# Kernel tuning notes

Hardware: AMD Instinct MI355X
Metric: run time of the kernel (lower is better)

## Reference

```python
import jax, jax.numpy as jnp
import numpy as np


def _resize_axis(x, axis, out_size):
    # PyTorch bilinear interpolate, align_corners=False, no antialias (half-pixel centers)
    in_size = x.shape[axis]
    src = (jnp.arange(out_size) + 0.5) * (in_size / out_size) - 0.5
    src = jnp.clip(src, 0.0, in_size - 1.0)
    lo = jnp.floor(src).astype(jnp.int32)
    hi = jnp.minimum(lo + 1, in_size - 1)
    w = (src - lo).astype(x.dtype)
    shp = [1] * x.ndim
    shp[axis] = out_size
    w = w.reshape(shp)
    return jnp.take(x, lo, axis=axis) * (1 - w) + jnp.take(x, hi, axis=axis) * w


def _bilinear(x, h, w):
    return _resize_axis(_resize_axis(x, 2, h), 3, w)


def _unfold3(x):
    # F.unfold(kernel_size=3, padding=1) -> [B, C, 9, H*W], kernel offsets row-major
    B, C, H, W = x.shape
    xp = jnp.pad(x, ((0, 0), (0, 0), (1, 1), (1, 1)))
    pats = jnp.stack([xp[:, :, dy:dy + H, dx:dx + W] for dy in range(3) for dx in range(3)], axis=2)
    return pats.reshape(B, C, 9, H * W)


def setup_inputs() -> dict:
    key = jax.random.key(0)
    ks = jax.random.split(key, 7)
    B, C, H, W = 4, 64, 192, 192
    return {
        "x": jax.random.normal(ks[0], (B, C, H, W), jnp.float32),
        "gn_weight": jnp.ones((C,), jnp.float32) + 0.1 * jax.random.normal(ks[1], (C,), jnp.float32),
        "gn_bias": 0.1 * jax.random.normal(ks[2], (C,), jnp.float32),
        "w1": jax.random.normal(ks[3], (2 * C, C), jnp.float32) / np.sqrt(C).astype(np.float32),
        "b1": 0.01 * jax.random.normal(ks[4], (2 * C,), jnp.float32),
        "w2": jax.random.normal(ks[5], (C, 2 * C), jnp.float32) / np.sqrt(2 * C).astype(np.float32),
        "b2": 0.01 * jax.random.normal(ks[6], (C,), jnp.float32),
    }


def reference(x, gn_weight, gn_bias, w1, b1, w2, b2):
    B, C, H, W = x.shape
    MIN_CONN, MAX_CONN, THRESHOLD, POWER = 1, 16, 0.3, 2
    KSQ = 9
    K_MAX = min(MAX_CONN, KSQ)
    EPS_NORM = 1e-12

    x_down = _bilinear(x, H // 2, W // 2)
    x_du = _bilinear(x_down, H, W)
    df = jnp.abs(x - x_du).sum(1, keepdims=True)            # [B,1,H,W]
    dmin = df.reshape(B, -1).min(1).reshape(B, 1, 1, 1)
    dmax = df.reshape(B, -1).max(1).reshape(B, 1, 1, 1)
    dfp = ((df - dmin) / (dmax - dmin + 1e-8)) ** POWER
    mask = (dfp > THRESHOLD).astype(x.dtype)
    conn = MIN_CONN + jnp.clip(jnp.round(dfp * (MAX_CONN - MIN_CONN)), 0) * mask
    counts = conn.reshape(B, H * W)                          # [B,HW]
    process = counts > 1

    # ---- per-pixel cosine similarity to 3x3 neighborhood ----
    patches = _unfold3(x)                                    # [B,C,9,HW]
    x_flat = x.reshape(B, C, H * W)
    xn = x_flat / jnp.maximum(jnp.linalg.norm(x_flat, axis=1, keepdims=True), EPS_NORM)
    pn = patches / jnp.maximum(jnp.linalg.norm(patches, axis=1, keepdims=True), EPS_NORM)
    sim = jnp.einsum('bcn,bckn->bkn', xn, pn)                # [B,9,HW]

    # ---- adaptive top-k (k = min(count, 9)) + exp-softmax weighted sum of raw patches ----
    order = jnp.argsort(-sim, axis=1)                        # descending over the 9 neighbors
    sim_s = jnp.take_along_axis(sim, order, axis=1)
    pat_s = jnp.take_along_axis(patches, jnp.broadcast_to(order[:, None], patches.shape), axis=2)
    k = jnp.minimum(counts, K_MAX)                           # [B,HW]
    keep = (jnp.arange(KSQ)[None, :, None] < k[:, None, :]).astype(x.dtype)
    wts = jnp.exp(sim_s) * keep
    wts = wts / jnp.maximum(wts.sum(1, keepdims=True), EPS_NORM)
    weighted = jnp.einsum('bckn,bkn->bcn', pat_s, wts)       # [B,C,HW]
    output = jnp.where(process[:, None, :], weighted, x_flat).reshape(B, C, H, W)

    # ---- GroupNorm(32, C) on identity ----
    G = 32
    xg = x.reshape(B, G, C // G, H, W)
    mu = xg.mean((2, 3, 4), keepdims=True)
    var = xg.var((2, 3, 4), keepdims=True)
    nx = ((xg - mu) / jnp.sqrt(var + 1e-5)).reshape(B, C, H, W)
    norm_x = nx * gn_weight[None, :, None, None] + gn_bias[None, :, None, None]

    enhanced = output + norm_x
    # ---- conv_ffn: 1x1 conv C->2C, ReLU, 1x1 conv 2C->C ----
    h1 = jax.nn.relu(jnp.einsum('oc,bchw->bohw', w1, enhanced) + b1[None, :, None, None])
    ffn = jnp.einsum('oc,bchw->bohw', w2, h1) + b2[None, :, None, None]
    return enhanced + ffn
```

## Files before the change

kernel.cpp:

```cpp
#include <hip/hip_runtime.h>
#include <hip/hip_bf16.h>

#define BB 4
#define CC 64
#define HH 192
#define WW 192
#define HWSZ (HH*WW)
#define HD 96
#define WD 96
#define GG 32
#define FTH 256
#define FPX 64
#define FBPB (HWSZ/FPX)
#define PBLK 128
#define BPB (HWSZ/PBLK)

typedef short short8 __attribute__((ext_vector_type(8)));
typedef float f32x4  __attribute__((ext_vector_type(4)));

struct __align__(8) f4p { float x, y, z, w; };

__device__ __forceinline__ unsigned short f2bf(float f) {
    unsigned u = __float_as_uint(f);
    return (unsigned short)((u + 0x7FFFu + ((u >> 16) & 1u)) >> 16);
}
__device__ __forceinline__ float bf2f(unsigned short s) {
    return __uint_as_float(((unsigned)s) << 16);
}
__device__ __forceinline__ unsigned pk2(float a, float b) {
    return (unsigned)f2bf(a) | ((unsigned)f2bf(b) << 16);
}
__device__ __forceinline__ short8 u4s8(uint4 u) {
    union { uint4 a; short8 b; } cvt; cvt.a = u; return cvt.b;
}

__device__ __forceinline__ int swz1152(int bid) {
    return (bid & 7) * 144 + (bid >> 3);
}
__device__ __forceinline__ int swz2304(int bid) {
    return (bid & 7) * 288 + (bid >> 3);
}

template<int XT>
__global__ __launch_bounds__(256) void k_pre(const float* __restrict__ x,
                                             const float* __restrict__ w1,
                                             const float* __restrict__ w2,
                                             unsigned* __restrict__ wf,
                                             float* __restrict__ df,
                                             float* __restrict__ nrm,
                                             float* __restrict__ gnacc,
                                             unsigned* __restrict__ mmmin,
                                             unsigned* __restrict__ mmmax,
                                             float* __restrict__ xt) {
    __shared__ float sgn[64];
    __shared__ float wmn[4], wmx[4];
    int tid = threadIdx.x;
    if (tid < 64) sgn[tid] = 0.f;
    __syncthreads();

    if (blockIdx.x < 16) {
        #pragma unroll
        for (int rep = 0; rep < 2; ++rep) {
            int i = blockIdx.x*512 + rep*256 + tid;
            if (i < 4096) {
                float2 v = ((const float2*)w1)[i];
                int j = i >> 5, cp = i & 31, c0 = cp << 1;
                int fi = ((j >> 4) << 1) + (c0 >> 5);
                int ln = (((c0 & 31) >> 3) << 4) + (j & 15);
                wf[fi*256 + ln*4 + (cp & 3)] = pk2(v.x, v.y);
            } else {
                int i2 = i - 4096;
                float2 v = ((const float2*)w2)[i2];
                int c = i2 >> 6, jp = i2 & 63, j0 = jp << 1;
                int fi = ((j0 >> 5) << 2) + (c >> 4);
                int ln = (((j0 & 31) >> 3) << 4) + (c & 15);
                wf[4096 + fi*256 + ln*4 + (jp & 3)] = pk2(v.x, v.y);
            }
        }
    }

    int virt = swz1152(blockIdx.x);
    int b = virt / BPB;
    int pb = (virt % BPB) * PBLK;
    int wave = tid >> 6, lane = tid & 63;
    int oct = lane >> 3, grp = lane & 7;
    int p0 = pb + wave*32 + grp*4;
    int h = p0 / WW, w0 = p0 % WW;

    float hs = fminf(fmaxf(0.5f*(float)h - 0.25f, 0.f), 95.f);
    int hl = (int)hs; int hh2 = min(hl+1, 95); float fh = hs - (float)hl;
    int r0 = 2*hl, r1 = 2*hh2;

    int t0 = min(max(w0/2 - 1, 0), 92);
    float wc[4][4];
    #pragma unroll
    for (int i = 0; i < 4; ++i) {
        float wsr = fminf(fmaxf(0.5f*(float)(w0+i) - 0.25f, 0.f), 95.f);
        int wl = (int)wsr; int wh = min(wl+1, 95); float fw = wsr - (float)wl;
        int kl = wl - t0, kh = wh - t0;
        #pragma unroll
        for (int k = 0; k < 4; ++k)
            wc[i][k] = ((k==kl) ? (1.f-fw) : 0.f) + ((k==kh) ? fw : 0.f);
    }

    const float* xb = x + (size_t)b*CC*HWSZ;
    float d[4]  = {0.f,0.f,0.f,0.f};
    float qn[4] = {0.f,0.f,0.f,0.f};
    float gs[4] = {0.f,0.f,0.f,0.f};
    float gq[4] = {0.f,0.f,0.f,0.f};
    #pragma unroll
    for (int half = 0; half < 2; ++half) {
        float4 xbuf[4];
        #pragma unroll
        for (int k4 = 0; k4 < 4; ++k4) {
            int cc = half*4 + k4;
            const float* pc = xb + (size_t)(oct*8 + cc)*HWSZ;
            float4 xc = *(const float4*)(pc + h*WW + w0);
            xbuf[k4] = xc;
            const float* pa = pc + r0*WW + 2*t0;
            const float* pq = pc + r1*WW + 2*t0;
            f4p A0 = *(const f4p*)(pa);       f4p A1 = *(const f4p*)(pa + 4);
            f4p B0 = *(const f4p*)(pa + WW);  f4p B1 = *(const f4p*)(pa + WW + 4);
            f4p C0 = *(const f4p*)(pq);       f4p C1 = *(const f4p*)(pq + 4);
            f4p D0 = *(const f4p*)(pq + WW);  f4p D1 = *(const f4p*)(pq + WW + 4);
            float ra[8] = {A0.x,A0.y,A0.z,A0.w, A1.x,A1.y,A1.z,A1.w};
            float rb[8] = {B0.x,B0.y,B0.z,B0.w, B1.x,B1.y,B1.z,B1.w};
            float rc[8] = {C0.x,C0.y,C0.z,C0.w, C1.x,C1.y,C1.z,C1.w};
            float rd[8] = {D0.x,D0.y,D0.z,D0.w, D1.x,D1.y,D1.z,D1.w};
            float T[4];
            #pragma unroll
            for (int k = 0; k < 4; ++k) {
                float xdA = 0.25f*((ra[2*k] + rb[2*k]) + (ra[2*k+1] + rb[2*k+1]));
                float xdB = 0.25f*((rc[2*k] + rd[2*k]) + (rc[2*k+1] + rd[2*k+1]));
                T[k] = (1.f-fh)*xdA + fh*xdB;
            }
            float xv[4] = {xc.x, xc.y, xc.z, xc.w};
            float sch = 0.f, qch = 0.f;
            #pragma unroll
            for (int i = 0; i < 4; ++i) {
                float du = (wc[i][0]*T[0] + wc[i][1]*T[1]) + (wc[i][2]*T[2] + wc[i][3]*T[3]);
                d[i] += fabsf(xv[i] - du);
                float x2 = xv[i]*xv[i];
                qn[i] += x2;
                sch += xv[i];
                qch += x2;
            }
            gs[cc>>1] += sch;
            gq[cc>>1] += qch;
        }
        if (XT) {
            #pragma unroll
            for (int i = 0; i < 4; ++i) {
                float4 v4 = make_float4(((const float*)&xbuf[0])[i],
                                        ((const float*)&xbuf[1])[i],
                                        ((const float*)&xbuf[2])[i],
                                        ((const float*)&xbuf[3])[i]);
                *(float4*)(xt + ((size_t)b*HWSZ + p0 + i)*CC + oct*8 + half*4) = v4;
            }
        }
    }
    #pragma unroll
    for (int o = 8; o <= 32; o <<= 1) {
        #pragma unroll
        for (int i = 0; i < 4; ++i) {
            d[i]  += __shfl_xor(d[i], o);
            qn[i] += __shfl_xor(qn[i], o);
        }
    }
    if (oct == 0) {
        *(float4*)(df  + (size_t)b*HWSZ + p0) = make_float4(d[0], d[1], d[2], d[3]);
        *(float4*)(nrm + (size_t)b*HWSZ + p0) =
            make_float4(sqrtf(qn[0]), sqrtf(qn[1]), sqrtf(qn[2]), sqrtf(qn[3]));
    }
    float mn = fminf(fminf(d[0], d[1]), fminf(d[2], d[3]));
    float mx = fmaxf(fmaxf(d[0], d[1]), fmaxf(d[2], d[3]));
    #pragma unroll
    for (int o = 1; o < 64; o <<= 1) {
        mn = fminf(mn, __shfl_xor(mn, o));
        mx = fmaxf(mx, __shfl_xor(mx, o));
    }
    if (lane == 0) { wmn[wave] = mn; wmx[wave] = mx; }
    #pragma unroll
    for (int o = 1; o <= 4; o <<= 1) {
        #pragma unroll
        for (int j = 0; j < 4; ++j) {
            gs[j] += __shfl_xor(gs[j], o);
            gq[j] += __shfl_xor(gq[j], o);
        }
    }
    if (grp == 0) {
        #pragma unroll
        for (int j = 0; j < 4; ++j) {
            atomicAdd(&sgn[2*(oct*4+j)],   gs[j]);
            atomicAdd(&sgn[2*(oct*4+j)+1], gq[j]);
        }
    }
    __syncthreads();
    if (tid < 64) atomicAdd(&gnacc[(size_t)b*64 + tid], sgn[tid]);
    if (tid == 0) {
        float bmn = fminf(fminf(wmn[0], wmn[1]), fminf(wmn[2], wmn[3]));
        float bmx = fmaxf(fmaxf(wmx[0], wmx[1]), fmaxf(wmx[2], wmx[3]));
        atomicMin(&mmmin[b], __float_as_uint(bmn));
        atomicMax(&mmmax[b], __float_as_uint(bmx));
    }
}

template<int XT>
__global__ __launch_bounds__(FTH, 4) void k_fused(const float* __restrict__ x,
                                                  const float* __restrict__ xt,
                                                  const float* __restrict__ df,
                                                  const float* __restrict__ nrm,
                                                  const unsigned* __restrict__ mmmin,
                                                  const unsigned* __restrict__ mmmax,
                                                  const float* __restrict__ gnacc,
                                                  const float* __restrict__ gw,
                                                  const float* __restrict__ gb,
                                                  const unsigned* __restrict__ wf,
                                                  const float* __restrict__ b1,
                                                  const float* __restrict__ b2,
                                                  float* __restrict__ out) {
    __shared__ __align__(16) unsigned char lds[12288];
    unsigned* se = (unsigned*)lds;
    unsigned* sh = (unsigned*)(lds + 8192);
    float* gnv = (float*)(lds + 8192);

    int tid = threadIdx.x;
    int wv = tid >> 6, lane = tid & 63;
    int q = lane >> 4, m = lane & 15;

    int virt = swz2304(blockIdx.x);
    int b = virt / FBPB;
    int pb = (virt % FBPB) * FPX;
    int pxl = wv*16 + m;
    int p = pb + pxl;
    int h = p / WW, w = p % WW;
    int cbase = q*16;

    if (tid < 32) {
        float n = 2.f*HWSZ;
        float mu  = gnacc[(size_t)b*64 + 2*tid] / n;
        float var = gnacc[(size_t)b*64 + 2*tid + 1] / n - mu*mu;
        gnv[2*tid]   = mu;
        gnv[2*tid+1] = rsqrtf(var + 1e-5f);
    }
    __syncthreads();

    float dmin = __uint_as_float(mmmin[b]);
    float dmax = __uint_as_float(mmmax[b]);
    float dfp = (df[b*HWSZ+p] - dmin) / (dmax - dmin + 1e-8f);
    dfp = dfp * dfp;
    bool maskv = dfp > 0.3f;
    float conn = 1.f + (maskv ? fmaxf(rintf(dfp * 15.f), 0.f) : 0.f);
    bool process = conn > 1.f;
    int kk = (int)fminf(conn, 9.f);

    const float* xb = x + (size_t)b*CC*HWSZ + p;
    const float* pt = xt + ((size_t)b*HWSZ + p)*CC + cbase;
    const int dhv[9] = {-1,-1,-1, 0,0,0, 1,1,1};
    const int dwv[9] = {-1, 0, 1,-1,0,1,-1,0,1};
    bool valid[9]; int offc[9];
    #pragma unroll
    for (int j = 0; j < 9; ++j) {
        int hn = h + dhv[j], wn = w + dwv[j];
        valid[j] = (hn >= 0) && (hn < HH) && (wn >= 0) && (wn < WW);
        offc[j] = valid[j] ? (dhv[j]*WW + dwv[j]) : 0;
    }
    float wtc[9];
    #pragma unroll
    for (int j = 0; j < 9; ++j) wtc[j] = 0.f;

    float xa[16];
    if (XT) {
        float4 X0 = *(const float4*)(pt + 0);
        float4 X1 = *(const float4*)(pt + 4);
        float4 X2 = *(const float4*)(pt + 8);
        float4 X3 = *(const float4*)(pt + 12);
        xa[0]=X0.x;  xa[1]=X0.y;  xa[2]=X0.z;  xa[3]=X0.w;
        xa[4]=X1.x;  xa[5]=X1.y;  xa[6]=X1.z;  xa[7]=X1.w;
        xa[8]=X2.x;  xa[9]=X2.y;  xa[10]=X2.z; xa[11]=X2.w;
        xa[12]=X3.x; xa[13]=X3.y; xa[14]=X3.z; xa[15]=X3.w;
    }

    if (process) {
        float dot[9];
        if (XT) {
            #pragma unroll
            for (int j = 0; j < 9; ++j) {
                const float* nb = pt + (ptrdiff_t)offc[j]*CC;
                float4 n0 = *(const float4*)(nb + 0);
                float4 n1 = *(const float4*)(nb + 4);
                float4 n2 = *(const float4*)(nb + 8);
                float4 n3 = *(const float4*)(nb + 12);
                float na[16];
                na[0]=n0.x;  na[1]=n0.y;  na[2]=n0.z;  na[3]=n0.w;
                na[4]=n1.x;  na[5]=n1.y;  na[6]=n1.z;  na[7]=n1.w;
                na[8]=n2.x;  na[9]=n2.y;  na[10]=n2.z; na[11]=n2.w;
                na[12]=n3.x; na[13]=n3.y; na[14]=n3.z; na[15]=n3.w;
                float s = 0.f;
                #pragma unroll
                for (int cc = 0; cc < 16; ++cc)
                    s += xa[cc] * na[cc];
                dot[j] = s;
            }
        } else {
            #pragma unroll
            for (int j = 0; j < 9; ++j) dot[j] = 0.f;
            #pragma unroll 4
            for (int cc = 0; cc < 16; ++cc) {
                const float* pc = xb + (size_t)(cbase + cc)*HWSZ;
                float xc = pc[0];
                #pragma unroll
                for (int j = 0; j < 9; ++j)
                    dot[j] += xc * pc[offc[j]];
            }
        }
        #pragma unroll
        for (int j = 0; j < 9; ++j) {
            dot[j] += __shfl_xor(dot[j], 16);
            dot[j] += __shfl_xor(dot[j], 32);
        }
        float nc = fmaxf(nrm[b*HWSZ+p], 1e-12f);
        float sim[9];
        #pragma unroll
        for (int j = 0; j < 9; ++j) {
            float nj = fmaxf(nrm[b*HWSZ+p+offc[j]], 1e-12f);
            sim[j] = valid[j] ? dot[j] / (nc * nj) : 0.f;
        }
        float S = 0.f;
        float wt[9];
        #pragma unroll
        for (int j = 0; j < 9; ++j) {
            int rank = 0;
            #pragma unroll
            for (int l = 0; l < 9; ++l)
                rank += (sim[l] > sim[j]) || (sim[l] == sim[j] && l < j);
            float ex = (rank < kk) ? expf(sim[j]) : 0.f;
            wt[j] = ex; S += ex;
        }
        float inv = 1.f / fmaxf(S, 1e-12f);
        #pragma unroll
        for (int j = 0; j < 9; ++j)
            wtc[j] = valid[j] ? wt[j] * inv : 0.f;
    }

    float e[16];
    if (XT) {
        float acc[16];
        if (process) {
            #pragma unroll
            for (int cc = 0; cc < 16; ++cc) acc[cc] = 0.f;
            #pragma unroll
            for (int j = 0; j < 9; ++j) {
                const float* nb = pt + (ptrdiff_t)offc[j]*CC;
                float4 n0 = *(const float4*)(nb + 0);
                float4 n1 = *(const float4*)(nb + 4);
                float4 n2 = *(const float4*)(nb + 8);
                float4 n3 = *(const float4*)(nb + 12);
                float wj = wtc[j];
                acc[0]  += wj*n0.x;  acc[1]  += wj*n0.y;
                acc[2]  += wj*n0.z;  acc[3]  += wj*n0.w;
                acc[4]  += wj*n1.x;  acc[5]  += wj*n1.y;
                acc[6]  += wj*n1.z;  acc[7]  += wj*n1.w;
                acc[8]  += wj*n2.x;  acc[9]  += wj*n2.y;
                acc[10] += wj*n2.z;  acc[11] += wj*n2.w;
                acc[12] += wj*n3.x;  acc[13] += wj*n3.y;
                acc[14] += wj*n3.z;  acc[15] += wj*n3.w;
            }
        }
        #pragma unroll
        for (int cc = 0; cc < 16; ++cc) {
            int c = cbase + cc;
            float xc = xa[cc];
            float oc = process ? acc[cc] : xc;
            int g = c >> 1;
            float mu = gnv[2*g], is = gnv[2*g+1];
            e[cc] = oc + (xc - mu) * is * gw[c] + gb[c];
        }
    } else {
        #pragma unroll 4
        for (int cc = 0; cc < 16; ++cc) {
            int c = cbase + cc;
            const float* pc = xb + (size_t)c*HWSZ;
            float xc = pc[0];
            float oc;
            if (process) {
                float a = 0.f;
                #pragma unroll
                for (int j = 0; j < 9; ++j)
                    a += wtc[j] * pc[offc[j]];
                oc = a;
            } else oc = xc;
            int g = c >> 1;
            float mu = gnv[2*g], is = gnv[2*g+1];
            e[cc] = oc + (xc - mu) * is * gw[c] + gb[c];
        }
    }

    {
        int kc = q >> 1, qo = q & 1;
        unsigned* dst = se + (wv*2 + kc)*256;
        int la = 32*qo + m;
        uint4 ua, ub;
        ua.x = pk2(e[0],e[1]);  ua.y = pk2(e[2],e[3]);
        ua.z = pk2(e[4],e[5]);  ua.w = pk2(e[6],e[7]);
        ub.x = pk2(e[8],e[9]);  ub.y = pk2(e[10],e[11]);
        ub.z = pk2(e[12],e[13]); ub.w = pk2(e[14],e[15]);
        *(uint4*)(dst + la*4)      = ua;
        *(uint4*)(dst + (la+16)*4) = ub;
    }
    __syncthreads();

    const unsigned* wf1g = wf;
    const unsigned* wf2g = wf + 4096;
    int n16 = m;
    float b1v[8], b2v[4];
    #pragma unroll
    for (int nt = 0; nt < 8; ++nt) b1v[nt] = b1[nt*16 + n16];
    #pragma unroll
    for (int n2 = 0; n2 < 4; ++n2) b2v[n2] = b2[n2*16 + n16];

    uint4 a0 = *(uint4*)(se + (wv*2+0)*256 + lane*4);
    uint4 a1 = *(uint4*)(se + (wv*2+1)*256 + lane*4);
    f32x4 D1[8];
    #pragma unroll
    for (int nt = 0; nt < 8; ++nt) D1[nt] = (f32x4){0.f,0.f,0.f,0.f};
    #pragma unroll
    for (int nt = 0; nt < 8; ++nt) {
        uint4 bk0 = *(const uint4*)(wf1g + (nt*2+0)*256 + lane*4);
        uint4 bk1 = *(const uint4*)(wf1g + (nt*2+1)*256 + lane*4);
        D1[nt] = __builtin_amdgcn_mfma_f32_16x16x32_bf16(u4s8(a0), u4s8(bk0), D1[nt], 0, 0, 0);
        D1[nt] = __builtin_amdgcn_mfma_f32_16x16x32_bf16(u4s8(a1), u4s8(bk1), D1[nt], 0, 0, 0);
    }
    f32x4 D2[4];
    #pragma unroll
    for (int n2 = 0; n2 < 4; ++n2) D2[n2] = (f32x4){0.f,0.f,0.f,0.f};
    unsigned* shwv = sh + wv*256;
    unsigned short* shw = (unsigned short*)shwv;
    for (int kc2 = 0; kc2 < 4; ++kc2) {
        #pragma unroll
        for (int h2 = 0; h2 < 2; ++h2) {
            int nt = kc2*2 + h2;
            #pragma unroll
            for (int r = 0; r < 4; ++r) {
                float hval = fmaxf(D1[nt][r] + b1v[nt], 0.f);
                int mrow = q*4 + r;
                int k = h2*16 + n16;
                shw[((k >> 3)*16 + mrow)*8 + (k & 7)] = f2bf(hval);
            }
        }
        uint4 ah = *(uint4*)(shwv + lane*4);
        #pragma unroll
        for (int n2 = 0; n2 < 4; ++n2) {
            uint4 bb = *(const uint4*)(wf2g + (kc2*4 + n2)*256 + lane*4);
            D2[n2] = __builtin_amdgcn_mfma_f32_16x16x32_bf16(u4s8(ah), u4s8(bb), D2[n2], 0, 0, 0);
        }
    }
    float vals[4][4];
    unsigned short* seu = (unsigned short*)se;
    #pragma unroll
    for (int n2 = 0; n2 < 4; ++n2) {
        int c = n2*16 + n16;
        int kc = c >> 5, qq = (c & 31) >> 3, jj = c & 7;
        #pragma unroll
        for (int r = 0; r < 4; ++r) {
            int pxt = q*4 + r;
            float resid = bf2f(seu[((wv*2+kc)*64 + qq*16 + pxt)*8 + jj]);
            vals[n2][r] = D2[n2][r] + resid + b2v[n2];
        }
    }
    __syncthreads();

    float* stg = (float*)lds;
    float* outb = out + (size_t)b*CC*HWSZ;
    #pragma unroll
    for (int g = 0; g < 2; ++g) {
        #pragma unroll
        for (int hn2 = 0; hn2 < 2; ++hn2) {
            int n2 = 2*g + hn2;
            int row = (n2 & 1)*16 + n16;
            float4 v4 = make_float4(vals[n2][0], vals[n2][1], vals[n2][2], vals[n2][3]);
            *(float4*)&stg[row*68 + wv*16 + q*4] = v4;
        }
        __syncthreads();
        #pragma unroll
        for (int rr = 0; rr < 2; ++rr) {
            int r0 = rr*16 + (tid >> 4);
            int px4 = (tid & 15) * 4;
            float4 v = *(float4*)&stg[r0*68 + px4];
            *(float4*)&outb[(size_t)(g*32 + r0)*HWSZ + pb + px4] = v;
        }
        if (g == 0) __syncthreads();
    }
}

extern "C" void kernel_launch(void* const* d_in, const int* in_sizes, int n_in,
                              void* d_out, int out_size, void* d_ws, size_t ws_size,
                              hipStream_t stream) {
    const float* x  = (const float*)d_in[0];
    const float* gw = (const float*)d_in[1];
    const float* gb = (const float*)d_in[2];
    const float* w1 = (const float*)d_in[3];
    const float* b1 = (const float*)d_in[4];
    const float* w2 = (const float*)d_in[5];
    const float* b2 = (const float*)d_in[6];
    float* out = (float*)d_out;

    float* df       = (float*)d_ws;
    float* nrm      = df + 147456;
    float* gnacc    = nrm + 147456;
    unsigned* mmmax = (unsigned*)(gnacc + 256);
    unsigned* mmmin = mmmax + 4;
    unsigned* wf    = mmmin + 4;
    float* xtp      = (float*)(wf + 8192);

    const size_t NEED = (size_t)(147456*2 + 256 + 8 + 8192 + (size_t)BB*CC*HWSZ) * 4;
    bool big = ws_size >= NEED;

    hipMemsetAsync(gnacc, 0, (256 + 4) * sizeof(float), stream);
    hipMemsetAsync(mmmin, 0xFF, 4 * sizeof(unsigned), stream);

    if (big) {
        k_pre<1>  <<<BB*BPB, 256, 0, stream>>>(x, w1, w2, wf, df, nrm, gnacc,
                                               mmmin, mmmax, xtp);
        k_fused<1><<<BB*FBPB, FTH, 0, stream>>>(x, xtp, df, nrm, mmmin, mmmax,
                                                gnacc, gw, gb, wf, b1, b2, out);
    } else {
        k_pre<0>  <<<BB*BPB, 256, 0, stream>>>(x, w1, w2, wf, df, nrm, gnacc,
                                               mmmin, mmmax, nullptr);
        k_fused<0><<<BB*FBPB, FTH, 0, stream>>>(x, nullptr, df, nrm, mmmin, mmmax,
                                                gnacc, gw, gb, wf, b1, b2, out);
    }
}
```

Before: 186.0 us.

## Compact processed pixels into a block-wide list to remove wave divergence

In the transposed-input path, each block builds a shared-memory list of pixels that need neighbor aggregation, using an atomic counter. The four waves then process that list densely, 16 pixels per iteration, and write the aggregated channels to an LDS buffer that each pixel's thread reads back. The aim is to avoid waves idling on masked-out lanes when only a sparse subset of pixels is processed. In exchange it adds extra barriers, LDS traffic and a larger LDS allocation, which may lower occupancy. The index h is reused from the thread's own pixel rather than recomputed from the list pixel, which could be wrong when a block spans row boundaries.

Result: slower. 195.7 us (+5.2%).

```diff
diff --git a/kernel.cpp b/kernel.cpp
--- a/kernel.cpp
+++ b/kernel.cpp
@@ -219,10 +219,14 @@
                                                   const float* __restrict__ b1,
                                                   const float* __restrict__ b2,
                                                   float* __restrict__ out) {
-    __shared__ __align__(16) unsigned char lds[12288];
-    unsigned* se = (unsigned*)lds;
-    unsigned* sh = (unsigned*)(lds + 8192);
-    float* gnv = (float*)(lds + 8192);
+    __shared__ __align__(16) unsigned char lds[22032];
+    float*    ocbuf = (float*)lds;
+    unsigned* se    = (unsigned*)lds;
+    unsigned* sh    = (unsigned*)(lds + 17408);
+    float*    gnv   = (float*)(lds + 17408);
+    int*      pflag = (int*)(lds + 21504);
+    int*      plist = (int*)(lds + 21760);
+    int*      npc   = (int*)(lds + 22016);
 
     int tid = threadIdx.x;
     int wv = tid >> 6, lane = tid & 63;
@@ -243,6 +247,7 @@
         gnv[2*tid]   = mu;
         gnv[2*tid+1] = rsqrtf(var + 1e-5f);
     }
+    if (tid == 32) *npc = 0;
     __syncthreads();
 
     float dmin = __uint_as_float(mmmin[b]);
@@ -254,21 +259,15 @@
     bool process = conn > 1.f;
     int kk = (int)fminf(conn, 9.f);
 
-    const float* xb = x + (size_t)b*CC*HWSZ + p;
-    const float* pt = xt + ((size_t)b*HWSZ + p)*CC + cbase;
     const int dhv[9] = {-1,-1,-1, 0,0,0, 1,1,1};
     const int dwv[9] = {-1, 0, 1,-1,0,1,-1,0,1};
-    bool valid[9]; int offc[9];
-    #pragma unroll
-    for (int j = 0; j < 9; ++j) {
-        int hn = h + dhv[j], wn = w + dwv[j];
-        valid[j] = (hn >= 0) && (hn < HH) && (wn >= 0) && (wn < WW);
-        offc[j] = valid[j] ? (dhv[j]*WW + dwv[j]) : 0;
-    }
-    float wtc[9];
-    #pragma unroll
-    for (int j = 0; j < 9; ++j) wtc[j] = 0.f;
-
+
+    if (XT && q == 0) {
+        pflag[pxl] = process ? kk : 0;
+        if (process) { int ix = atomicAdd(npc, 1); plist[ix] = pxl; }
+    }
+
+    const float* pt = XT ? (xt + ((size_t)b*HWSZ + p)*CC + cbase) : nullptr;
     float xa[16];
     if (XT) {
         float4 X0 = *(const float4*)(pt + 0);
@@ -280,29 +279,148 @@
         xa[8]=X2.x;  xa[9]=X2.y;  xa[10]=X2.z; xa[11]=X2.w;
         xa[12]=X3.x; xa[13]=X3.y; xa[14]=X3.z; xa[15]=X3.w;
     }
-
-    if (process) {
-        float dot[9];
-        if (XT) {
+    __syncthreads();
+
+    float e[16];
+    if (XT) {
+        int NP = *npc;
+        for (int it = wv; it*16 < NP; it += 4) {
+            int li = it*16 + m;
+            bool act = li < NP;
+            int pl = act ? plist[li] : 0;
+            int kk2 = act ? pflag[pl] : 9;
+            int p2 = pb + pl;
+            int w2 = p2 % WW;
+            bool valid2[9]; int offc2[9];
             #pragma unroll
             for (int j = 0; j < 9; ++j) {
-                const float* nb = pt + (ptrdiff_t)offc[j]*CC;
-                float4 n0 = *(const float4*)(nb + 0);
-                float4 n1 = *(const float4*)(nb + 4);
-                float4 n2 = *(const float4*)(nb + 8);
-                float4 n3 = *(const float4*)(nb + 12);
-                float na[16];
-                na[0]=n0.x;  na[1]=n0.y;  na[2]=n0.z;  na[3]=n0.w;
-                na[4]=n1.x;  na[5]=n1.y;  na[6]=n1.z;  na[7]=n1.w;
-                na[8]=n2.x;  na[9]=n2.y;  na[10]=n2.z; na[11]=n2.w;
-                na[12]=n3.x; na[13]=n3.y; na[14]=n3.z; na[15]=n3.w;
-                float s = 0.f;
-                #pragma unroll
-                for (int cc = 0; cc < 16; ++cc)
-                    s += xa[cc] * na[cc];
-                dot[j] = s;
-            }
+                int hn = h + dhv[j], wn = w2 + dwv[j];
+                valid2[j] = (hn >= 0) && (hn < HH) && (wn >= 0) && (wn < WW);
+                offc2[j] = valid2[j] ? (dhv[j]*WW + dwv[j]) : 0;
+            }
+            const float* pt2 = xt + ((size_t)b*HWSZ + p2)*CC + cbase;
+            if (act) {
+                float4 Y0 = *(const float4*)(pt2 + 0);
+                float4 Y1 = *(const float4*)(pt2 + 4);
+                float4 Y2 = *(const float4*)(pt2 + 8);
+                float4 Y3 = *(const float4*)(pt2 + 12);
+                float xa2[16];
+                xa2[0]=Y0.x;  xa2[1]=Y0.y;  xa2[2]=Y0.z;  xa2[3]=Y0.w;
+                xa2[4]=Y1.x;  xa2[5]=Y1.y;  xa2[6]=Y1.z;  xa2[7]=Y1.w;
+                xa2[8]=Y2.x;  xa2[9]=Y2.y;  xa2[10]=Y2.z; xa2[11]=Y2.w;
+                xa2[12]=Y3.x; xa2[13]=Y3.y; xa2[14]=Y3.z; xa2[15]=Y3.w;
+                float dot[9];
+                #pragma unroll
+                for (int j = 0; j < 9; ++j) {
+                    const float* nb = pt2 + (ptrdiff_t)offc2[j]*CC;
+                    float4 n0 = *(const float4*)(nb + 0);
+                    float4 n1 = *(const float4*)(nb + 4);
+                    float4 n2 = *(const float4*)(nb + 8);
+                    float4 n3 = *(const float4*)(nb + 12);
+                    float na[16];
+                    na[0]=n0.x;  na[1]=n0.y;  na[2]=n0.z;  na[3]=n0.w;
+                    na[4]=n1.x;  na[5]=n1.y;  na[6]=n1.z;  na[7]=n1.w;
+                    na[8]=n2.x;  na[9]=n2.y;  na[10]=n2.z; na[11]=n2.w;
+                    na[12]=n3.x; na[13]=n3.y; na[14]=n3.z; na[15]=n3.w;
+                    float s = 0.f;
+                    #pragma unroll
+                    for (int cc = 0; cc < 16; ++cc)
+                        s += xa2[cc] * na[cc];
+                    dot[j] = s;
+                }
+                #pragma unroll
+                for (int j = 0; j < 9; ++j) {
+                    dot[j] += __shfl_xor(dot[j], 16);
+                    dot[j] += __shfl_xor(dot[j], 32);
+                }
+                float nc = fmaxf(nrm[b*HWSZ+p2], 1e-12f);
+                float sim[9];
+                #pragma unroll
+                for (int j = 0; j < 9; ++j) {
+                    float nj = fmaxf(nrm[b*HWSZ+p2+offc2[j]], 1e-12f);
+                    sim[j] = valid2[j] ? dot[j] / (nc * nj) : 0.f;
+                }
+                float S = 0.f, wt[9];
+                #pragma unroll
+                for (int j = 0; j < 9; ++j) {
+                    int rank = 0;
+                    #pragma unroll
+                    for (int l = 0; l < 9; ++l)
+                        rank += (sim[l] > sim[j]) || (sim[l] == sim[j] && l < j);
+                    float ex = (rank < kk2) ? expf(sim[j]) : 0.f;
+                    wt[j] = ex; S += ex;
+                }
+                float inv = 1.f / fmaxf(S, 1e-12f);
+                float wtc2[9];
+                #pragma unroll
+                for (int j = 0; j < 9; ++j)
+                    wtc2[j] = valid2[j] ? wt[j] * inv : 0.f;
+                float acc[16];
+                #pragma unroll
+                for (int cc = 0; cc < 16; ++cc) acc[cc] = 0.f;
+                #pragma unroll
+                for (int j = 0; j < 9; ++j) {
+                    const float* nb = pt2 + (ptrdiff_t)offc2[j]*CC;
+                    float4 n0 = *(const float4*)(nb + 0);
+                    float4 n1 = *(const float4*)(nb + 4);
+                    float4 n2 = *(const float4*)(nb + 8);
+                    float4 n3 = *(const float4*)(nb + 12);
+                    float wj = wtc2[j];
+                    acc[0]  += wj*n0.x;  acc[1]  += wj*n0.y;
+                    acc[2]  += wj*n0.z;  acc[3]  += wj*n0.w;
+                    acc[4]  += wj*n1.x;  acc[5]  += wj*n1.y;
+                    acc[6]  += wj*n1.z;  acc[7]  += wj*n1.w;
+                    acc[8]  += wj*n2.x;  acc[9]  += wj*n2.y;
+                    acc[10] += wj*n2.z;  acc[11] += wj*n2.w;
+                    acc[12] += wj*n3.x;  acc[13] += wj*n3.y;
+                    acc[14] += wj*n3.z;  acc[15] += wj*n3.w;
+                }
+                float* od = ocbuf + pl*68 + cbase;
+                *(float4*)(od + 0)  = make_float4(acc[0], acc[1], acc[2], acc[3]);
+                *(float4*)(od + 4)  = make_float4(acc[4], acc[5], acc[6], acc[7]);
+                *(float4*)(od + 8)  = make_float4(acc[8], acc[9], acc[10], acc[11]);
+                *(float4*)(od + 12) = make_float4(acc[12], acc[13], acc[14], acc[15]);
+            }
+        }
+        __syncthreads();
+
+        float oc16[16];
+        if (process) {
+            const float* os = ocbuf + pxl*68 + cbase;
+            float4 O0 = *(const float4*)(os + 0);
+            float4 O1 = *(const float4*)(os + 4);
+            float4 O2 = *(const float4*)(os + 8);
+            float4 O3 = *(const float4*)(os + 12);
+            oc16[0]=O0.x;  oc16[1]=O0.y;  oc16[2]=O0.z;  oc16[3]=O0.w;
+            oc16[4]=O1.x;  oc16[5]=O1.y;  oc16[6]=O1.z;  oc16[7]=O1.w;
+            oc16[8]=O2.x;  oc16[9]=O2.y;  oc16[10]=O2.z; oc16[11]=O2.w;
+            oc16[12]=O3.x; oc16[13]=O3.y; oc16[14]=O3.z; oc16[15]=O3.w;
         } else {
+            #pragma unroll
+            for (int cc = 0; cc < 16; ++cc) oc16[cc] = xa[cc];
+        }
+        #pragma unroll
+        for (int cc = 0; cc < 16; ++cc) {
+            int c = cbase + cc;
+            float xc = xa[cc];
+            int g = c >> 1;
+            float mu = gnv[2*g], is = gnv[2*g+1];
+            e[cc] = oc16[cc] + (xc - mu) * is * gw[c] + gb[c];
+        }
+    } else {
+        const float* xb = x + (size_t)b*CC*HWSZ + p;
+        bool valid[9]; int offc[9];
+        #pragma unroll
+        for (int j = 0; j < 9; ++j) {
+            int hn = h + dhv[j], wn = w + dwv[j];
+            valid[j] = (hn >= 0) && (hn < HH) && (wn >= 0) && (wn < WW);
+            offc[j] = valid[j] ? (dhv[j]*WW + dwv[j]) : 0;
+        }
+        float wtc[9];
+        #pragma unroll
+        for (int j = 0; j < 9; ++j) wtc[j] = 0.f;
+        if (process) {
+            float dot[9];
             #pragma unroll
             for (int j = 0; j < 9; ++j) dot[j] = 0.f;
             #pragma unroll 4
@@ -313,70 +431,33 @@
                 for (int j = 0; j < 9; ++j)
                     dot[j] += xc * pc[offc[j]];
             }
-        }
-        #pragma unroll
-        for (int j = 0; j < 9; ++j) {
-            dot[j] += __shfl_xor(dot[j], 16);
-            dot[j] += __shfl_xor(dot[j], 32);
-        }
-        float nc = fmaxf(nrm[b*HWSZ+p], 1e-12f);
-        float sim[9];
-        #pragma unroll
-        for (int j = 0; j < 9; ++j) {
-            float nj = fmaxf(nrm[b*HWSZ+p+offc[j]], 1e-12f);
-            sim[j] = valid[j] ? dot[j] / (nc * nj) : 0.f;
-        }
-        float S = 0.f;
-        float wt[9];
-        #pragma unroll
-        for (int j = 0; j < 9; ++j) {
-            int rank = 0;
-            #pragma unroll
-            for (int l = 0; l < 9; ++l)
-                rank += (sim[l] > sim[j]) || (sim[l] == sim[j] && l < j);
-            float ex = (rank < kk) ? expf(sim[j]) : 0.f;
-            wt[j] = ex; S += ex;
-        }
-        float inv = 1.f / fmaxf(S, 1e-12f);
-        #pragma unroll
-        for (int j = 0; j < 9; ++j)
-            wtc[j] = valid[j] ? wt[j] * inv : 0.f;
-    }
-
-    float e[16];
-    if (XT) {
-        float acc[16];
-        if (process) {
-            #pragma unroll
-            for (int cc = 0; cc < 16; ++cc) acc[cc] = 0.f;
             #pragma unroll
             for (int j = 0; j < 9; ++j) {
-                const float* nb = pt + (ptrdiff_t)offc[j]*CC;
-                float4 n0 = *(const float4*)(nb + 0);
-                float4 n1 = *(const float4*)(nb + 4);
-                float4 n2 = *(const float4*)(nb + 8);
-                float4 n3 = *(const float4*)(nb + 12);
-                float wj = wtc[j];
-                acc[0]  += wj*n0.x;  acc[1]  += wj*n0.y;
-                acc[2]  += wj*n0.z;  acc[3]  += wj*n0.w;
-                acc[4]  += wj*n1.x;  acc[5]  += wj*n1.y;
-                acc[6]  += wj*n1.z;  acc[7]  += wj*n1.w;
-                acc[8]  += wj*n2.x;  acc[9]  += wj*n2.y;
-                acc[10] += wj*n2.z;  acc[11] += wj*n2.w;
-                acc[12] += wj*n3.x;  acc[13] += wj*n3.y;
-                acc[14] += wj*n3.z;  acc[15] += wj*n3.w;
-            }
-        }
-        #pragma unroll
-        for (int cc = 0; cc < 16; ++cc) {
-            int c = cbase + cc;
-            float xc = xa[cc];
-            float oc = process ? acc[cc] : xc;
-            int g = c >> 1;
-            float mu = gnv[2*g], is = gnv[2*g+1];
-            e[cc] = oc + (xc - mu) * is * gw[c] + gb[c];
-        }
-    } else {
+                dot[j] += __shfl_xor(dot[j], 16);
+                dot[j] += __shfl_xor(dot[j], 32);
+            }
+            float nc = fmaxf(nrm[b*HWSZ+p], 1e-12f);
+            float sim[9];
+            #pragma unroll
+            for (int j = 0; j < 9; ++j) {
+                float nj = fmaxf(nrm[b*HWSZ+p+offc[j]], 1e-12f);
+                sim[j] = valid[j] ? dot[j] / (nc * nj) : 0.f;
+            }
+            float S = 0.f, wt[9];
+            #pragma unroll
+            for (int j = 0; j < 9; ++j) {
+                int rank = 0;
+                #pragma unroll
+                for (int l = 0; l < 9; ++l)
+                    rank += (sim[l] > sim[j]) || (sim[l] == sim[j] && l < j);
+                float ex = (rank < kk) ? expf(sim[j]) : 0.f;
+                wt[j] = ex; S += ex;
+            }
+            float inv = 1.f / fmaxf(S, 1e-12f);
+            #pragma unroll
+            for (int j = 0; j < 9; ++j)
+                wtc[j] = valid[j] ? wt[j] * inv : 0.f;
+        }
         #pragma unroll 4
         for (int cc = 0; cc < 16; ++cc) {
             int c = cbase + cc;
@@ -395,6 +476,7 @@
             e[cc] = oc + (xc - mu) * is * gw[c] + gb[c];
         }
     }
+    __syncthreads();
 
     {
         int kc = q >> 1, qo = q & 1;
```
